# Optimization experiments

Hardware: AMD Instinct MI355X
Metric: run time of the kernel (lower is better)

The kernel has to match this reference:

```python
import jax, jax.numpy as jnp
import numpy as np

NUM_USERS = 100000
NUM_ITEMS = 50000
N_NODES = NUM_USERS + NUM_ITEMS
EMB_DIM = 64
N_LAYERS = 3
NNZ = 4800000


def setup_inputs() -> dict:
    key = jax.random.key(0)
    k1, k2, k3, k4, k5 = jax.random.split(key, 5)
    user_emb = jax.random.normal(k1, (NUM_USERS, EMB_DIM), dtype=jnp.float32)
    item_emb = jax.random.normal(k2, (NUM_ITEMS, EMB_DIM), dtype=jnp.float32)
    adj_rows = jax.random.randint(k3, (NNZ,), 0, N_NODES, dtype=jnp.int32)
    adj_cols = jax.random.randint(k4, (NNZ,), 0, N_NODES, dtype=jnp.int32)
    adj_vals = jax.random.uniform(k5, (NNZ,), dtype=jnp.float32)
    return {"user_emb": user_emb, "item_emb": item_emb,
            "adj_rows": adj_rows, "adj_cols": adj_cols, "adj_vals": adj_vals}


def _spmm(rows, cols, vals, x):
    # COO SpMM: out[r] += vals * x[c]   (gather + weighted segment-sum)
    return jax.ops.segment_sum(vals[:, None] * x[cols], rows,
                               num_segments=N_NODES)


def reference(user_emb, item_emb, adj_rows, adj_cols, adj_vals):
    all_emb = jnp.concatenate([user_emb, item_emb], axis=0)  # [N, D]
    acc = all_emb
    cur = all_emb
    for _ in range(N_LAYERS):
        cur = _spmm(adj_rows, adj_cols, adj_vals, cur)
        acc = acc + cur
    out = acc / jnp.float32(N_LAYERS + 1)  # mean over stacked layer outputs
    users = out[:NUM_USERS]
    items = out[NUM_USERS:]
    return users, items
```

## Files before the change

### kernel.cpp

```cpp
#include <hip/hip_runtime.h>
#include <hip/hip_fp16.h>

#define NUM_USERS 100000
#define NUM_ITEMS 50000
#define N_NODES   150000
#define EMB_DIM   64
#define NNZ       4800000
#define N_LAYERS  3

#define TILE_ROWS 256
#define TILE_SHIFT 8
#define NTILES    ((N_NODES + TILE_ROWS - 1) / TILE_ROWS)
#define COL_BITS  18
#define COL_MASK  ((1 << COL_BITS) - 1)
#define VAL_BITS  14
#define VAL_MASK  ((1 << VAL_BITS) - 1)

static constexpr size_t TOTAL = (size_t)N_NODES * EMB_DIM;

__global__ void lgcn_init_h(const float4* __restrict__ user_emb,
                            const float4* __restrict__ item_emb,
                            uint2* __restrict__ cur16) {
    size_t i = (size_t)blockIdx.x * blockDim.x + threadIdx.x;
    const size_t n4 = TOTAL / 4;
    if (i >= n4) return;
    const size_t ub4 = (size_t)NUM_USERS * EMB_DIM / 4;
    float4 v = (i < ub4) ? user_emb[i] : item_emb[i - ub4];
    __half2 h0 = __floats2half2_rn(v.x, v.y);
    __half2 h1 = __floats2half2_rn(v.z, v.w);
    uint2 u;
    u.x = *reinterpret_cast<unsigned int*>(&h0);
    u.y = *reinterpret_cast<unsigned int*>(&h1);
    cur16[i] = u;
}

__global__ void tile_hist(const int* __restrict__ rows, int* __restrict__ tileCnt) {
    __shared__ int h[NTILES];
    for (int i = threadIdx.x; i < NTILES; i += blockDim.x) h[i] = 0;
    __syncthreads();
    for (size_t e = (size_t)blockIdx.x * blockDim.x + threadIdx.x; e < NNZ;
         e += (size_t)gridDim.x * blockDim.x)
        atomicAdd(&h[rows[e] >> TILE_SHIFT], 1);
    __syncthreads();
    for (int i = threadIdx.x; i < NTILES; i += blockDim.x) {
        int c = h[i];
        if (c) atomicAdd(&tileCnt[i], c);
    }
}

__global__ void tile_scan(const int* __restrict__ tileCnt,
                          int* __restrict__ tile_ptr,
                          int* __restrict__ tile_cursor,
                          int* __restrict__ row_ptr) {
    __shared__ int s[1024];
    int t = threadIdx.x;
    int v = (t < NTILES) ? tileCnt[t] : 0;
    s[t] = v;
    __syncthreads();
    for (int off = 1; off < 1024; off <<= 1) {
        int add = (t >= off) ? s[t - off] : 0;
        __syncthreads();
        s[t] += add;
        __syncthreads();
    }
    if (t < NTILES) {
        int ex = s[t] - v;
        tile_ptr[t] = ex;
        tile_cursor[t] = ex;
    }
    if (t == 0) {
        tile_ptr[NTILES] = NNZ;
        row_ptr[N_NODES] = NNZ;
    }
}

#define BKT_BLK 1024
#define EPB     8192

__global__ __launch_bounds__(BKT_BLK) void
edge_bucket(const int* __restrict__ rows, const int* __restrict__ cols,
            const float* __restrict__ vals, int* __restrict__ tile_cursor,
            int2* __restrict__ ebuf1) {
    __shared__ int2 stage[EPB];
    __shared__ int  dstIdx[EPB];
    __shared__ int  hcur[NTILES];
    __shared__ int  lbase[NTILES];
    __shared__ int  gbase[NTILES];

    int tid = threadIdx.x;
    size_t blockStart = (size_t)blockIdx.x * EPB;

    int r[8]; int c[8]; float v[8];
    for (int i = tid; i < NTILES; i += BKT_BLK) hcur[i] = 0;
    __syncthreads();

    #pragma unroll
    for (int k = 0; k < 8; k++) {
        size_t e = blockStart + (size_t)k * BKT_BLK + tid;
        if (e < NNZ) {
            r[k] = rows[e]; c[k] = cols[e]; v[k] = vals[e];
            atomicAdd(&hcur[r[k] >> TILE_SHIFT], 1);
        } else r[k] = -1;
    }
    __syncthreads();

    int cnt = (tid < NTILES) ? hcur[tid] : 0;
    for (int off = 1; off < 1024; off <<= 1) {
        int add = (tid >= off && tid < NTILES) ? hcur[tid - off] : 0;
        __syncthreads();
        if (tid < NTILES) hcur[tid] += add;
        __syncthreads();
    }
    if (tid < NTILES) {
        int ex = hcur[tid] - cnt;
        lbase[tid] = ex;
        gbase[tid] = cnt ? atomicAdd(&tile_cursor[tid], cnt) : 0;
    }
    __syncthreads();
    if (tid < NTILES) hcur[tid] = lbase[tid];
    __syncthreads();

    #pragma unroll
    for (int k = 0; k < 8; k++) {
        if (r[k] >= 0) {
            int t = r[k] >> TILE_SHIFT;
            int slot = atomicAdd(&hcur[t], 1);
            stage[slot] = make_int2(((r[k] & (TILE_ROWS - 1)) << COL_BITS) | c[k],
                                    __float_as_int(v[k]));
            dstIdx[slot] = gbase[t] + (slot - lbase[t]);
        }
    }
    __syncthreads();

    int total = (int)min((size_t)EPB, (size_t)NNZ - blockStart);
    for (int i = tid; i < total; i += BKT_BLK)
        ebuf1[dstIdx[i]] = stage[i];
}

#define RS_BLK 512

__global__ __launch_bounds__(RS_BLK) void
row_sort(const int2* __restrict__ ebuf1, const int* __restrict__ tile_ptr,
         int* __restrict__ row_ptr, unsigned int* __restrict__ epack) {
    __shared__ int hist[TILE_ROWS];
    __shared__ int cur256[TILE_ROWS];
    int tid = threadIdx.x;
    int tile = blockIdx.x;
    int s  = tile_ptr[tile];
    int e1 = tile_ptr[tile + 1];

    if (tid < TILE_ROWS) hist[tid] = 0;
    __syncthreads();

    for (int i = s + tid; i < e1; i += RS_BLK)
        atomicAdd(&hist[(unsigned)ebuf1[i].x >> COL_BITS], 1);
    __syncthreads();

    int v = (tid < TILE_ROWS) ? hist[tid] : 0;
    for (int off = 1; off < TILE_ROWS; off <<= 1) {
        int add = (tid >= off && tid < TILE_ROWS) ? hist[tid - off] : 0;
        __syncthreads();
        if (tid < TILE_ROWS) hist[tid] += add;
        __syncthreads();
    }
    if (tid < TILE_ROWS) {
        int excl = hist[tid] - v;
        int rowG = tile * TILE_ROWS + tid;
        if (rowG < N_NODES) row_ptr[rowG] = s + excl;
        cur256[tid] = s + excl;
    }
    __syncthreads();

    for (int i = s + tid; i < e1; i += RS_BLK) {
        int2 m = ebuf1[i];
        int r = (unsigned)m.x >> COL_BITS;
        int pos = atomicAdd(&cur256[r], 1);
        unsigned int col = (unsigned)m.x & COL_MASK;
        float val = __int_as_float(m.y);
        int q = (int)(val * 16384.0f + 0.5f);
        if (q > VAL_MASK) q = VAL_MASK;
        epack[pos] = (col << VAL_BITS) | (unsigned)q;
    }
}

__device__ __forceinline__ void fma8(uint4 xv, float v, float* a) {
    const __half2* h = reinterpret_cast<const __half2*>(&xv);
    #pragma unroll
    for (int k = 0; k < 4; k++) {
        float2 f = __half22float2(h[k]);
        a[2*k]   = fmaf(v, f.x, a[2*k]);
        a[2*k+1] = fmaf(v, f.y, a[2*k+1]);
    }
}

template <int FINAL>
__global__ void lgcn_spmm_csr_h8(const int* __restrict__ row_ptr,
                                 const unsigned int* __restrict__ edges,
                                 const uint4* __restrict__ x16v,
                                 uint4* __restrict__ y16v,
                                 const float4* __restrict__ user_emb,
                                 const float4* __restrict__ item_emb,
                                 const uint4* __restrict__ y1v,
                                 const uint4* __restrict__ y2v,
                                 float4* __restrict__ outv) {
    int wid = blockIdx.x * (blockDim.x >> 6) + (threadIdx.x >> 6);
    if (wid >= N_NODES) return;
    int lane = threadIdx.x & 63;
    int g = lane >> 3;
    int t = lane & 7;
    int e  = row_ptr[wid];
    int e1 = row_ptr[wid + 1];
    float a[8] = {0.f,0.f,0.f,0.f,0.f,0.f,0.f,0.f};
    const float inv = 1.0f / 16384.0f;

    for (; e + 8 <= e1; e += 8) {
        unsigned int m = edges[e + g];
        uint4 xv = x16v[(size_t)(m >> VAL_BITS) * 8 + t];
        fma8(xv, (float)(m & VAL_MASK) * inv, a);
    }
    int rem = e1 - e;
    if (g < rem) {
        unsigned int m = edges[e + g];
        uint4 xv = x16v[(size_t)(m >> VAL_BITS) * 8 + t];
        fma8(xv, (float)(m & VAL_MASK) * inv, a);
    }

    #pragma unroll
    for (int k = 0; k < 8; k++) a[k] += __shfl_xor(a[k], 8);
    #pragma unroll
    for (int k = 0; k < 8; k++) a[k] += __shfl_xor(a[k], 16);
    #pragma unroll
    for (int k = 0; k < 8; k++) a[k] += __shfl_xor(a[k], 32);

    if (lane < 8) {
        if (!FINAL) {
            __half2 h[4];
            #pragma unroll
            for (int k = 0; k < 4; k++) h[k] = __floats2half2_rn(a[2*k], a[2*k+1]);
            uint4 u = *reinterpret_cast<uint4*>(h);
            y16v[(size_t)wid * 8 + t] = u;
        } else {
            const float4* inp = (wid < NUM_USERS)
                ? (user_emb + (size_t)wid * 16)
                : (item_emb + (size_t)(wid - NUM_USERS) * 16);
            uint4 u1 = y1v[(size_t)wid * 8 + t];
            uint4 u2 = y2v[(size_t)wid * 8 + t];
            const __half2* h1 = reinterpret_cast<const __half2*>(&u1);
            const __half2* h2 = reinterpret_cast<const __half2*>(&u2);
            float4 o0 = inp[2*t];
            float4 o1 = inp[2*t + 1];
            float s[8];
            #pragma unroll
            for (int k = 0; k < 4; k++) {
                float2 f1 = __half22float2(h1[k]);
                float2 f2 = __half22float2(h2[k]);
                s[2*k]   = f1.x + f2.x;
                s[2*k+1] = f1.y + f2.y;
            }
            o0.x = (o0.x + s[0] + a[0]) * 0.25f;
            o0.y = (o0.y + s[1] + a[1]) * 0.25f;
            o0.z = (o0.z + s[2] + a[2]) * 0.25f;
            o0.w = (o0.w + s[3] + a[3]) * 0.25f;
            o1.x = (o1.x + s[4] + a[4]) * 0.25f;
            o1.y = (o1.y + s[5] + a[5]) * 0.25f;
            o1.z = (o1.z + s[6] + a[6]) * 0.25f;
            o1.w = (o1.w + s[7] + a[7]) * 0.25f;
            outv[(size_t)wid * 16 + 2*t]     = o0;
            outv[(size_t)wid * 16 + 2*t + 1] = o1;
        }
    }
}

__global__ void lgcn_init_f(const float4* __restrict__ user_emb,
                            const float4* __restrict__ item_emb,
                            float4* __restrict__ cur,
                            float4* __restrict__ acc) {
    size_t i = (size_t)blockIdx.x * blockDim.x + threadIdx.x;
    const size_t n4 = TOTAL / 4;
    if (i >= n4) return;
    const size_t ub4 = (size_t)NUM_USERS * EMB_DIM / 4;
    float4 v = (i < ub4) ? user_emb[i] : item_emb[i - ub4];
    cur[i] = v;
    acc[i] = v;
}

__global__ void lgcn_spmm_scatter(const int* __restrict__ rows,
                                  const int* __restrict__ cols,
                                  const float* __restrict__ vals,
                                  const float* __restrict__ x,
                                  float* __restrict__ y) {
    size_t t = (size_t)blockIdx.x * blockDim.x + threadIdx.x;
    if (t >= (size_t)NNZ * EMB_DIM) return;
    int e = (int)(t >> 6);
    int d = (int)(t & 63);
    atomicAdd(&y[(size_t)rows[e] * EMB_DIM + d], vals[e] * x[(size_t)cols[e] * EMB_DIM + d]);
}

__global__ void lgcn_accum(float4* __restrict__ acc, const float4* __restrict__ nxt, float scale) {
    size_t i = (size_t)blockIdx.x * blockDim.x + threadIdx.x;
    const size_t n4 = TOTAL / 4;
    if (i >= n4) return;
    float4 a = acc[i]; float4 b = nxt[i];
    a.x = (a.x + b.x) * scale; a.y = (a.y + b.y) * scale;
    a.z = (a.z + b.z) * scale; a.w = (a.w + b.w) * scale;
    acc[i] = a;
}

extern "C" void kernel_launch(void* const* d_in, const int* in_sizes, int n_in,
                              void* d_out, int out_size, void* d_ws, size_t ws_size,
                              hipStream_t stream) {
    const float* user_emb = (const float*)d_in[0];
    const float* item_emb = (const float*)d_in[1];
    const int*   rows     = (const int*)d_in[2];
    const int*   cols     = (const int*)d_in[3];
    const float* vals     = (const float*)d_in[4];
    float* out = (float*)d_out;

    const int BLK = 256;
    const size_t n4 = TOTAL / 4;
    dim3 g_init((n4 + BLK - 1) / BLK);

    char* p = (char*)d_ws;
    unsigned int* epack = (unsigned int*)p;  p += (size_t)NNZ * sizeof(unsigned int);
    __half* y1 = (__half*)p;
    int2*   ebuf1 = (int2*)p;                p += (size_t)NNZ * sizeof(int2);
    __half* y2 = y1 + TOTAL;
    __half* cur16 = (__half*)p;              p += TOTAL * sizeof(__half);
    __half* y3 = (__half*)p;                 p += TOTAL * sizeof(__half);
    int*    tileCnt = (int*)p;               p += (size_t)NTILES * sizeof(int);
    int*    tile_ptr = (int*)p;              p += (size_t)(NTILES + 1) * sizeof(int);
    int*    tile_cursor = (int*)p;           p += (size_t)NTILES * sizeof(int);
    int*    row_ptr = (int*)p;               p += (size_t)(N_NODES + 1) * sizeof(int);
    size_t needed = (size_t)(p - (char*)d_ws);

    if (ws_size < needed) {
        float* fcur = (float*)d_ws;
        float* fnxt = fcur + TOTAL;
        lgcn_init_f<<<g_init, BLK, 0, stream>>>((const float4*)user_emb, (const float4*)item_emb,
                                                (float4*)fcur, (float4*)out);
        const size_t st = (size_t)NNZ * EMB_DIM;
        dim3 g_scat((st + BLK - 1) / BLK);
        for (int l = 0; l < N_LAYERS; ++l) {
            hipMemsetAsync(fnxt, 0, TOTAL * sizeof(float), stream);
            lgcn_spmm_scatter<<<g_scat, BLK, 0, stream>>>(rows, cols, vals, fcur, fnxt);
            float scale = (l == N_LAYERS - 1) ? (1.0f / (N_LAYERS + 1)) : 1.0f;
            lgcn_accum<<<g_init, BLK, 0, stream>>>((float4*)out, (const float4*)fnxt, scale);
            float* t = fcur; fcur = fnxt; fnxt = t;
        }
        return;
    }

    hipMemsetAsync(tileCnt, 0, (size_t)NTILES * sizeof(int), stream);
    tile_hist<<<1024, 256, 0, stream>>>(rows, tileCnt);
    tile_scan<<<1, 1024, 0, stream>>>(tileCnt, tile_ptr, tile_cursor, row_ptr);
    int nBuckBlocks = (NNZ + EPB - 1) / EPB;
    edge_bucket<<<nBuckBlocks, BKT_BLK, 0, stream>>>(rows, cols, vals, tile_cursor, ebuf1);
    row_sort<<<NTILES, RS_BLK, 0, stream>>>(ebuf1, tile_ptr, row_ptr, epack);

    lgcn_init_h<<<g_init, BLK, 0, stream>>>((const float4*)user_emb, (const float4*)item_emb,
                                            (uint2*)cur16);

    const int WAVES_PER_BLK = BLK / 64;
    dim3 g_spmm((N_NODES + WAVES_PER_BLK - 1) / WAVES_PER_BLK);
    lgcn_spmm_csr_h8<0><<<g_spmm, BLK, 0, stream>>>(row_ptr, epack,
        (const uint4*)cur16, (uint4*)y1, nullptr, nullptr, nullptr, nullptr, nullptr);
    lgcn_spmm_csr_h8<0><<<g_spmm, BLK, 0, stream>>>(row_ptr, epack,
        (const uint4*)y1, (uint4*)y2, nullptr, nullptr, nullptr, nullptr, nullptr);
    lgcn_spmm_csr_h8<1><<<g_spmm, BLK, 0, stream>>>(row_ptr, epack,
        (const uint4*)y2, (uint4*)y3,
        (const float4*)user_emb, (const float4*)item_emb,
        (const uint4*)y1, (const uint4*)y2, (float4*)out);
}
```

Baseline: 410.2 us.

## Drop histogram pass with padded tile buckets and accumulate SpMM in half2

Removes the separate tile histogram pass. Edges are bucketed directly into fixed-size padded per-tile regions, and the scan of tile counts now runs after bucketing. Edge values are stored as fp16 bit patterns, and the SpMM accumulates with half2 FMAs and half2 shuffles instead of fp32. The final layer reads the input embeddings from the fp16 copy rather than the fp32 originals. Non-temporal loads and stores are also added. This trades accuracy (fp16 accumulation over about 32 edges per row, fp16 layer-0 input) for less ALU and memory work, and the padded buckets overflow if any tile receives more than PAD edges.

```diff
diff --git a/kernel.cpp b/kernel.cpp
--- a/kernel.cpp
+++ b/kernel.cpp
@@ -15,8 +15,12 @@
 #define COL_MASK  ((1 << COL_BITS) - 1)
 #define VAL_BITS  14
 #define VAL_MASK  ((1 << VAL_BITS) - 1)
+#define PAD       10240
 
 static constexpr size_t TOTAL = (size_t)N_NODES * EMB_DIM;
+
+typedef unsigned int uv4 __attribute__((ext_vector_type(4)));
+typedef long long    ll1;
 
 __global__ void lgcn_init_h(const float4* __restrict__ user_emb,
                             const float4* __restrict__ item_emb,
@@ -34,46 +38,6 @@
     cur16[i] = u;
 }
 
-__global__ void tile_hist(const int* __restrict__ rows, int* __restrict__ tileCnt) {
-    __shared__ int h[NTILES];
-    for (int i = threadIdx.x; i < NTILES; i += blockDim.x) h[i] = 0;
-    __syncthreads();
-    for (size_t e = (size_t)blockIdx.x * blockDim.x + threadIdx.x; e < NNZ;
-         e += (size_t)gridDim.x * blockDim.x)
-        atomicAdd(&h[rows[e] >> TILE_SHIFT], 1);
-    __syncthreads();
-    for (int i = threadIdx.x; i < NTILES; i += blockDim.x) {
-        int c = h[i];
-        if (c) atomicAdd(&tileCnt[i], c);
-    }
-}
-
-__global__ void tile_scan(const int* __restrict__ tileCnt,
-                          int* __restrict__ tile_ptr,
-                          int* __restrict__ tile_cursor,
-                          int* __restrict__ row_ptr) {
-    __shared__ int s[1024];
-    int t = threadIdx.x;
-    int v = (t < NTILES) ? tileCnt[t] : 0;
-    s[t] = v;
-    __syncthreads();
-    for (int off = 1; off < 1024; off <<= 1) {
-        int add = (t >= off) ? s[t - off] : 0;
-        __syncthreads();
-        s[t] += add;
-        __syncthreads();
-    }
-    if (t < NTILES) {
-        int ex = s[t] - v;
-        tile_ptr[t] = ex;
-        tile_cursor[t] = ex;
-    }
-    if (t == 0) {
-        tile_ptr[NTILES] = NNZ;
-        row_ptr[N_NODES] = NNZ;
-    }
-}
-
 #define BKT_BLK 1024
 #define EPB     8192
 
@@ -98,7 +62,9 @@
     for (int k = 0; k < 8; k++) {
         size_t e = blockStart + (size_t)k * BKT_BLK + tid;
         if (e < NNZ) {
-            r[k] = rows[e]; c[k] = cols[e]; v[k] = vals[e];
+            r[k] = __builtin_nontemporal_load(&rows[e]);
+            c[k] = __builtin_nontemporal_load(&cols[e]);
+            v[k] = __builtin_nontemporal_load(&vals[e]);
             atomicAdd(&hcur[r[k] >> TILE_SHIFT], 1);
         } else r[k] = -1;
     }
@@ -114,7 +80,7 @@
     if (tid < NTILES) {
         int ex = hcur[tid] - cnt;
         lbase[tid] = ex;
-        gbase[tid] = cnt ? atomicAdd(&tile_cursor[tid], cnt) : 0;
+        gbase[tid] = cnt ? (tid * PAD + atomicAdd(&tile_cursor[tid], cnt)) : 0;
     }
     __syncthreads();
     if (tid < NTILES) hcur[tid] = lbase[tid];
@@ -137,6 +103,27 @@
         ebuf1[dstIdx[i]] = stage[i];
 }
 
+__global__ void tile_scan(const int* __restrict__ counts,
+                          int* __restrict__ tile_ptr,
+                          int* __restrict__ row_ptr) {
+    __shared__ int s[1024];
+    int t = threadIdx.x;
+    int v = (t < NTILES) ? counts[t] : 0;
+    s[t] = v;
+    __syncthreads();
+    for (int off = 1; off < 1024; off <<= 1) {
+        int add = (t >= off) ? s[t - off] : 0;
+        __syncthreads();
+        s[t] += add;
+        __syncthreads();
+    }
+    if (t < NTILES) tile_ptr[t] = s[t] - v;
+    if (t == 0) {
+        tile_ptr[NTILES] = NNZ;
+        row_ptr[N_NODES] = NNZ;
+    }
+}
+
 #define RS_BLK 512
 
 __global__ __launch_bounds__(RS_BLK) void
@@ -146,14 +133,19 @@
     __shared__ int cur256[TILE_ROWS];
     int tid = threadIdx.x;
     int tile = blockIdx.x;
-    int s  = tile_ptr[tile];
-    int e1 = tile_ptr[tile + 1];
+    int base_in = tile * PAD;
+    int obase = tile_ptr[tile];
+    int cnt = tile_ptr[tile + 1] - obase;
+    const ll1* eb64 = reinterpret_cast<const ll1*>(ebuf1);
 
     if (tid < TILE_ROWS) hist[tid] = 0;
     __syncthreads();
 
-    for (int i = s + tid; i < e1; i += RS_BLK)
-        atomicAdd(&hist[(unsigned)ebuf1[i].x >> COL_BITS], 1);
+    for (int i = tid; i < cnt; i += RS_BLK) {
+        ll1 raw = __builtin_nontemporal_load(&eb64[base_in + i]);
+        unsigned int mx = (unsigned int)(unsigned long long)raw;
+        atomicAdd(&hist[mx >> COL_BITS], 1);
+    }
     __syncthreads();
 
     int v = (tid < TILE_ROWS) ? hist[tid] : 0;
@@ -166,43 +158,33 @@
     if (tid < TILE_ROWS) {
         int excl = hist[tid] - v;
         int rowG = tile * TILE_ROWS + tid;
-        if (rowG < N_NODES) row_ptr[rowG] = s + excl;
-        cur256[tid] = s + excl;
-    }
-    __syncthreads();
-
-    for (int i = s + tid; i < e1; i += RS_BLK) {
-        int2 m = ebuf1[i];
-        int r = (unsigned)m.x >> COL_BITS;
+        if (rowG < N_NODES) row_ptr[rowG] = obase + excl;
+        cur256[tid] = obase + excl;
+    }
+    __syncthreads();
+
+    for (int i = tid; i < cnt; i += RS_BLK) {
+        ll1 raw = __builtin_nontemporal_load(&eb64[base_in + i]);
+        unsigned int mx = (unsigned int)(unsigned long long)raw;
+        unsigned int my = (unsigned int)((unsigned long long)raw >> 32);
+        int r = mx >> COL_BITS;
         int pos = atomicAdd(&cur256[r], 1);
-        unsigned int col = (unsigned)m.x & COL_MASK;
-        float val = __int_as_float(m.y);
-        int q = (int)(val * 16384.0f + 0.5f);
-        if (q > VAL_MASK) q = VAL_MASK;
-        epack[pos] = (col << VAL_BITS) | (unsigned)q;
-    }
-}
-
-__device__ __forceinline__ void fma8(uint4 xv, float v, float* a) {
-    const __half2* h = reinterpret_cast<const __half2*>(&xv);
-    #pragma unroll
-    for (int k = 0; k < 4; k++) {
-        float2 f = __half22float2(h[k]);
-        a[2*k]   = fmaf(v, f.x, a[2*k]);
-        a[2*k+1] = fmaf(v, f.y, a[2*k+1]);
+        unsigned int col = mx & COL_MASK;
+        unsigned int hb = (unsigned)__half_as_ushort(__float2half_rn(__uint_as_float(my)));
+        if (hb > (unsigned)VAL_MASK) hb = VAL_MASK;
+        epack[pos] = (col << VAL_BITS) | hb;
     }
 }
 
 template <int FINAL>
-__global__ void lgcn_spmm_csr_h8(const int* __restrict__ row_ptr,
-                                 const unsigned int* __restrict__ edges,
-                                 const uint4* __restrict__ x16v,
-                                 uint4* __restrict__ y16v,
-                                 const float4* __restrict__ user_emb,
-                                 const float4* __restrict__ item_emb,
-                                 const uint4* __restrict__ y1v,
-                                 const uint4* __restrict__ y2v,
-                                 float4* __restrict__ outv) {
+__global__ void lgcn_spmm_h8(const int* __restrict__ row_ptr,
+                             const unsigned int* __restrict__ edges,
+                             const uint4* __restrict__ x16v,
+                             uint4* __restrict__ y16v,
+                             const uint4* __restrict__ x0v,
+                             const uint4* __restrict__ y1v,
+                             const uint4* __restrict__ y2v,
+                             float4* __restrict__ outv) {
     int wid = blockIdx.x * (blockDim.x >> 6) + (threadIdx.x >> 6);
     if (wid >= N_NODES) return;
     int lane = threadIdx.x & 63;
@@ -210,61 +192,77 @@
     int t = lane & 7;
     int e  = row_ptr[wid];
     int e1 = row_ptr[wid + 1];
-    float a[8] = {0.f,0.f,0.f,0.f,0.f,0.f,0.f,0.f};
-    const float inv = 1.0f / 16384.0f;
+
+    __half2 a0 = __float2half2_rn(0.0f), a1 = a0, a2 = a0, a3 = a0;
 
     for (; e + 8 <= e1; e += 8) {
-        unsigned int m = edges[e + g];
+        unsigned int m = __builtin_nontemporal_load(&edges[e + g]);
         uint4 xv = x16v[(size_t)(m >> VAL_BITS) * 8 + t];
-        fma8(xv, (float)(m & VAL_MASK) * inv, a);
+        unsigned int vv = (m & VAL_MASK);
+        vv |= (vv << 16);
+        __half2 vh = *reinterpret_cast<__half2*>(&vv);
+        const __half2* xh = reinterpret_cast<const __half2*>(&xv);
+        a0 = __hfma2(xh[0], vh, a0);
+        a1 = __hfma2(xh[1], vh, a1);
+        a2 = __hfma2(xh[2], vh, a2);
+        a3 = __hfma2(xh[3], vh, a3);
     }
     int rem = e1 - e;
     if (g < rem) {
-        unsigned int m = edges[e + g];
+        unsigned int m = __builtin_nontemporal_load(&edges[e + g]);
         uint4 xv = x16v[(size_t)(m >> VAL_BITS) * 8 + t];
-        fma8(xv, (float)(m & VAL_MASK) * inv, a);
+        unsigned int vv = (m & VAL_MASK);
+        vv |= (vv << 16);
+        __half2 vh = *reinterpret_cast<__half2*>(&vv);
+        const __half2* xh = reinterpret_cast<const __half2*>(&xv);
+        a0 = __hfma2(xh[0], vh, a0);
+        a1 = __hfma2(xh[1], vh, a1);
+        a2 = __hfma2(xh[2], vh, a2);
+        a3 = __hfma2(xh[3], vh, a3);
     }
 
     #pragma unroll
-    for (int k = 0; k < 8; k++) a[k] += __shfl_xor(a[k], 8);
-    #pragma unroll
-    for (int k = 0; k < 8; k++) a[k] += __shfl_xor(a[k], 16);
-    #pragma unroll
-    for (int k = 0; k < 8; k++) a[k] += __shfl_xor(a[k], 32);
+    for (int mask = 8; mask <= 32; mask <<= 1) {
+        unsigned int u;
+        u = __shfl_xor(*reinterpret_cast<unsigned int*>(&a0), mask);
+        a0 = __hadd2(a0, *reinterpret_cast<__half2*>(&u));
+        u = __shfl_xor(*reinterpret_cast<unsigned int*>(&a1), mask);
+        a1 = __hadd2(a1, *reinterpret_cast<__half2*>(&u));
+        u = __shfl_xor(*reinterpret_cast<unsigned int*>(&a2), mask);
+        a2 = __hadd2(a2, *reinterpret_cast<__half2*>(&u));
+        u = __shfl_xor(*reinterpret_cast<unsigned int*>(&a3), mask);
+        a3 = __hadd2(a3, *reinterpret_cast<__half2*>(&u));
+    }
 
     if (lane < 8) {
+        size_t idx = (size_t)wid * 8 + t;
         if (!FINAL) {
-            __half2 h[4];
-            #pragma unroll
-            for (int k = 0; k < 4; k++) h[k] = __floats2half2_rn(a[2*k], a[2*k+1]);
-            uint4 u = *reinterpret_cast<uint4*>(h);
-            y16v[(size_t)wid * 8 + t] = u;
+            uv4 u;
+            u.x = *reinterpret_cast<unsigned int*>(&a0);
+            u.y = *reinterpret_cast<unsigned int*>(&a1);
+            u.z = *reinterpret_cast<unsigned int*>(&a2);
+            u.w = *reinterpret_cast<unsigned int*>(&a3);
+            __builtin_nontemporal_store(u, reinterpret_cast<uv4*>(&y16v[idx]));
         } else {
-            const float4* inp = (wid < NUM_USERS)
-                ? (user_emb + (size_t)wid * 16)
-                : (item_emb + (size_t)(wid - NUM_USERS) * 16);
-            uint4 u1 = y1v[(size_t)wid * 8 + t];
-            uint4 u2 = y2v[(size_t)wid * 8 + t];
+            uint4 ux = x0v[idx];
+            uint4 u1 = y1v[idx];
+            uint4 u2 = y2v[idx];
+            const __half2* hx = reinterpret_cast<const __half2*>(&ux);
             const __half2* h1 = reinterpret_cast<const __half2*>(&u1);
             const __half2* h2 = reinterpret_cast<const __half2*>(&u2);
-            float4 o0 = inp[2*t];
-            float4 o1 = inp[2*t + 1];
-            float s[8];
+            __half2 av[4] = {a0, a1, a2, a3};
+            float o[8];
             #pragma unroll
             for (int k = 0; k < 4; k++) {
+                float2 fx = __half22float2(hx[k]);
                 float2 f1 = __half22float2(h1[k]);
                 float2 f2 = __half22float2(h2[k]);
-                s[2*k]   = f1.x + f2.x;
-                s[2*k+1] = f1.y + f2.y;
+                float2 fa = __half22float2(av[k]);
+                o[2*k]   = (fx.x + f1.x + f2.x + fa.x) * 0.25f;
+                o[2*k+1] = (fx.y + f1.y + f2.y + fa.y) * 0.25f;
             }
-            o0.x = (o0.x + s[0] + a[0]) * 0.25f;
-            o0.y = (o0.y + s[1] + a[1]) * 0.25f;
-            o0.z = (o0.z + s[2] + a[2]) * 0.25f;
-            o0.w = (o0.w + s[3] + a[3]) * 0.25f;
-            o1.x = (o1.x + s[4] + a[4]) * 0.25f;
-            o1.y = (o1.y + s[5] + a[5]) * 0.25f;
-            o1.z = (o1.z + s[6] + a[6]) * 0.25f;
-            o1.w = (o1.w + s[7] + a[7]) * 0.25f;
+            float4 o0 = make_float4(o[0], o[1], o[2], o[3]);
+            float4 o1 = make_float4(o[4], o[5], o[6], o[7]);
             outv[(size_t)wid * 16 + 2*t]     = o0;
             outv[(size_t)wid * 16 + 2*t + 1] = o1;
         }
@@ -323,11 +321,9 @@
     char* p = (char*)d_ws;
     unsigned int* epack = (unsigned int*)p;  p += (size_t)NNZ * sizeof(unsigned int);
     __half* y1 = (__half*)p;
-    int2*   ebuf1 = (int2*)p;                p += (size_t)NNZ * sizeof(int2);
+    int2*   ebuf1 = (int2*)p;                p += (size_t)NTILES * PAD * sizeof(int2);
     __half* y2 = y1 + TOTAL;
     __half* cur16 = (__half*)p;              p += TOTAL * sizeof(__half);
-    __half* y3 = (__half*)p;                 p += TOTAL * sizeof(__half);
-    int*    tileCnt = (int*)p;               p += (size_t)NTILES * sizeof(int);
     int*    tile_ptr = (int*)p;              p += (size_t)(NTILES + 1) * sizeof(int);
     int*    tile_cursor = (int*)p;           p += (size_t)NTILES * sizeof(int);
     int*    row_ptr = (int*)p;               p += (size_t)(N_NODES + 1) * sizeof(int);
@@ -350,11 +346,10 @@
         return;
     }
 
-    hipMemsetAsync(tileCnt, 0, (size_t)NTILES * sizeof(int), stream);
-    tile_hist<<<1024, 256, 0, stream>>>(rows, tileCnt);
-    tile_scan<<<1, 1024, 0, stream>>>(tileCnt, tile_ptr, tile_cursor, row_ptr);
+    hipMemsetAsync(tile_cursor, 0, (size_t)NTILES * sizeof(int), stream);
     int nBuckBlocks = (NNZ + EPB - 1) / EPB;
     edge_bucket<<<nBuckBlocks, BKT_BLK, 0, stream>>>(rows, cols, vals, tile_cursor, ebuf1);
+    tile_scan<<<1, 1024, 0, stream>>>(tile_cursor, tile_ptr, row_ptr);
     row_sort<<<NTILES, RS_BLK, 0, stream>>>(ebuf1, tile_ptr, row_ptr, epack);
 
     lgcn_init_h<<<g_init, BLK, 0, stream>>>((const float4*)user_emb, (const float4*)item_emb,
@@ -362,12 +357,11 @@
 
     const int WAVES_PER_BLK = BLK / 64;
     dim3 g_spmm((N_NODES + WAVES_PER_BLK - 1) / WAVES_PER_BLK);
-    lgcn_spmm_csr_h8<0><<<g_spmm, BLK, 0, stream>>>(row_ptr, epack,
-        (const uint4*)cur16, (uint4*)y1, nullptr, nullptr, nullptr, nullptr, nullptr);
-    lgcn_spmm_csr_h8<0><<<g_spmm, BLK, 0, stream>>>(row_ptr, epack,
-        (const uint4*)y1, (uint4*)y2, nullptr, nullptr, nullptr, nullptr, nullptr);
-    lgcn_spmm_csr_h8<1><<<g_spmm, BLK, 0, stream>>>(row_ptr, epack,
-        (const uint4*)y2, (uint4*)y3,
-        (const float4*)user_emb, (const float4*)item_emb,
-        (const uint4*)y1, (const uint4*)y2, (float4*)out);
-}
+    lgcn_spmm_h8<0><<<g_spmm, BLK, 0, stream>>>(row_ptr, epack,
+        (const uint4*)cur16, (uint4*)y1, nullptr, nullptr, nullptr, nullptr);
+    lgcn_spmm_h8<0><<<g_spmm, BLK, 0, stream>>>(row_ptr, epack,
+        (const uint4*)y1, (uint4*)y2, nullptr, nullptr, nullptr, nullptr);
+    lgcn_spmm_h8<1><<<g_spmm, BLK, 0, stream>>>(row_ptr, epack,
+        (const uint4*)y2, nullptr,
+        (const uint4*)cur16, (const uint4*)y1, (const uint4*)y2, (float4*)out);
+}
```

New measurement: 461.7 us. 1.13x slower.
